# Kernel tuning notes

Measured on AMD Instinct MI355X. Metric: run time of the kernel, lower is better.

## Reference

```python
import jax, jax.numpy as jnp
import numpy as np

B, C, H, W = 256, 200, 32, 32


def setup_inputs() -> dict:
    key = jax.random.key(0)
    x = jax.random.normal(key, (B, C, H, W), dtype=jnp.float32)
    # exact init of the torch nn.Parameter: log(3.2 / c^2) * ones(1,1)
    temperature = jnp.log(3.2 / (C * C)) * jnp.ones((1, 1), dtype=jnp.float32)
    return {"x": x, "temperature": temperature}


def reference(x, temperature):
    b, c, h, w = x.shape
    xf = x.reshape(b, c, h * w)                     # (B, c, hw)
    # Gram matrix x @ x^T  -> (B, c, c)
    G = jnp.einsum('bcm,bdm->bcd', xf, xf)
    # diagonal of G = squared norms per band  -> (B, c)
    d = jnp.einsum('bcm,bcm->bc', xf, xf)
    # I_M @ (G*I) puts d_j in every row; (G*I) @ I_M puts d_i in every column
    dcov = d[:, None, :] + d[:, :, None] - 2.0 * G  # (B, c, c)
    dcov = jnp.maximum(dcov, 0.0)
    dcov = jnp.sqrt(jnp.exp(temperature)[0, 0] * dcov + 1e-5)
    # double centering: dcov@I_M/c = row means, I_M@dcov/c = col means,
    # I_M@dcov@I_M/c^2 = global mean (per batch element)
    row_mean = jnp.mean(dcov, axis=2, keepdims=True)
    col_mean = jnp.mean(dcov, axis=1, keepdims=True)
    tot_mean = jnp.mean(dcov, axis=(1, 2), keepdims=True)
    return -(dcov - row_mean - col_mean + tot_mean)
```

## Files before the change

### kernel.cpp

```cpp
#include <hip/hip_runtime.h>
#include <hip/hip_bf16.h>

typedef __bf16 bf16x8 __attribute__((ext_vector_type(8)));
typedef float  f32x4  __attribute__((ext_vector_type(4)));

#define C_DIM   200
#define HW_DIM  1024
#define NT      13
#define PADC    208
#define BK      64
#define NKC     16
#define ROWB    128
#define TILEB   (PADC*ROWB)
#define SLAB    (PADC*HW_DIM)

#define GLD16(gp, lp) __builtin_amdgcn_global_load_lds(                      \
    (const __attribute__((address_space(1))) unsigned int*)(gp),             \
    (__attribute__((address_space(3))) unsigned int*)(lp), 16, 0, 0)

__global__ __launch_bounds__(832, 4)
void spectral_corr_kernel(const float* __restrict__ x,
                          const float* __restrict__ temp,
                          float* __restrict__ out,
                          __hip_bfloat16* __restrict__ ws)
{
  __shared__ __align__(16) char sA[2][TILEB];
  __shared__ float d_lds[PADC];
  __shared__ float rs_lds[PADC];

  const int tid = threadIdx.x;
  const int b   = blockIdx.x;
  const int w   = tid >> 6;
  const int l   = tid & 63;
  const int g   = l >> 4;
  const int c   = l & 15;

  const float*    xb = x  + (size_t)b * (C_DIM * HW_DIM);
  __hip_bfloat16* wb = ws + (size_t)b * SLAB;

  for (int base = tid*8; base < C_DIM*HW_DIM; base += 832*8){
    float4 a0 = *(const float4*)(xb + base);
    float4 a1 = *(const float4*)(xb + base + 4);
    bf16x8 v;
    v[0]=(__bf16)a0.x; v[1]=(__bf16)a0.y; v[2]=(__bf16)a0.z; v[3]=(__bf16)a0.w;
    v[4]=(__bf16)a1.x; v[5]=(__bf16)a1.y; v[6]=(__bf16)a1.z; v[7]=(__bf16)a1.w;
    *reinterpret_cast<bf16x8*>(wb + base) = v;
  }
  __syncthreads();

  const float et = expf(temp[0]);

  const int si = l >> 3;
  const int sc = (l & 7) ^ si;
  const int i0 = 2*w, i1 = 2*w + 1;
  const __hip_bfloat16* gs0 = wb + (size_t)(8*i0 + si)*HW_DIM + sc*8;
  const __hip_bfloat16* gs1 = wb + (size_t)(8*i1 + si)*HW_DIM + sc*8;

  f32x4 acc[NT];
  #pragma unroll
  for (int j=0;j<NT;++j) acc[j] = (f32x4){0.f,0.f,0.f,0.f};

  GLD16(gs0, &sA[0][i0*1024]);
  GLD16(gs1, &sA[0][i1*1024]);
  __syncthreads();

  const int swz = (c & 7) << 4;
  const int rb0 = c*ROWB + ((     g*16) ^ swz);
  const int rb1 = c*ROWB + ((64 + g*16) ^ swz);

  for (int kc = 0; kc < NKC; ++kc){
    const char* bufc = sA[kc & 1];
    if (kc+1 < NKC){
      char* bufn = sA[(kc+1)&1];
      GLD16(gs0 + (kc+1)*BK, &bufn[i0*1024]);
      GLD16(gs1 + (kc+1)*BK, &bufn[i1*1024]);
    }
    #pragma unroll
    for (int s = 0; s < 2; ++s){
      const char* p = bufc + (s ? rb1 : rb0);
      bf16x8 fw = *reinterpret_cast<const bf16x8*>(p + w*2048);
      #pragma unroll
      for (int j = 0; j < NT; ++j){
        bf16x8 fj = *reinterpret_cast<const bf16x8*>(p + j*2048);
        acc[j] = __builtin_amdgcn_mfma_f32_16x16x32_bf16(fw, fj, acc[j], 0, 0, 0);
      }
    }
    __syncthreads();
  }

  #pragma unroll
  for (int j=0;j<NT;++j){
    if (j == w){
      #pragma unroll
      for (int i=0;i<4;++i)
        if (c == g*4 + i) d_lds[j*16 + c] = acc[j][i];
    }
  }
  __syncthreads();

  float dr[4];
  #pragma unroll
  for (int i=0;i<4;++i) dr[i] = d_lds[w*16 + g*4 + i];
  float rsum[4] = {0.f,0.f,0.f,0.f};
  #pragma unroll
  for (int j=0;j<NT;++j){
    const float dc = d_lds[j*16 + c];
    const bool cv  = (j*16 + c) < C_DIM;
    #pragma unroll
    for (int i=0;i<4;++i){
      float v = dr[i] + dc - 2.0f*acc[j][i];
      v = fmaxf(v, 0.0f);
      v = sqrtf(fmaf(et, v, 1e-5f));
      acc[j][i] = v;
      if (cv) rsum[i] += v;
    }
  }
  #pragma unroll
  for (int m=1;m<16;m<<=1){
    #pragma unroll
    for (int i=0;i<4;++i) rsum[i] += __shfl_xor(rsum[i], m, 64);
  }
  if (c == 0){
    #pragma unroll
    for (int i=0;i<4;++i) rs_lds[w*16 + g*4 + i] = rsum[i];
  }
  __syncthreads();

  float tot = 0.f;
  for (int r=0;r<C_DIM;++r) tot += rs_lds[r];
  const float inv  = 1.0f/(float)C_DIM;
  const float totm = tot*inv*inv;

  float* ob = out + b*(C_DIM*C_DIM);
  float rmr[4];
  #pragma unroll
  for (int i=0;i<4;++i) rmr[i] = rs_lds[w*16 + g*4 + i]*inv;
  #pragma unroll
  for (int j=0;j<NT;++j){
    const int col = j*16 + c;
    if (col < C_DIM){
      const float rmc = rs_lds[col]*inv;
      #pragma unroll
      for (int i=0;i<4;++i){
        const int row = w*16 + g*4 + i;
        if (row < C_DIM)
          ob[row*C_DIM + col] = rmr[i] + rmc - totm - acc[j][i];
      }
    }
  }
}

extern "C" void kernel_launch(void* const* d_in, const int* in_sizes, int n_in,
                              void* d_out, int out_size, void* d_ws, size_t ws_size,
                              hipStream_t stream) {
  const float* x    = (const float*)d_in[0];
  const float* temp = (const float*)d_in[1];
  float* out        = (float*)d_out;
  __hip_bfloat16* ws = (__hip_bfloat16*)d_ws;
  spectral_corr_kernel<<<dim3(256), dim3(832), 0, stream>>>(x, temp, out, ws);
}
```

Before: 354.0 us.

## Interleave fp32-to-bf16 conversion with the MFMA K-loop two chunks ahead

Previously the whole per-batch slab was converted from fp32 to bf16 into workspace before any matrix work began, behind one block-wide barrier. Now only the first two K-chunks are converted up front. Each loop iteration loads the fp32 data for chunk kc+2 into registers before its MFMAs, then packs and stores it to workspace after them, so global-memory latency overlaps with tensor-core compute. This raises register pressure and relies on the existing per-iteration barrier to make workspace writes visible before the later global-to-LDS loads read them.

```diff
diff --git a/kernel.cpp b/kernel.cpp
--- a/kernel.cpp
+++ b/kernel.cpp
@@ -17,6 +17,13 @@
 #define GLD16(gp, lp) __builtin_amdgcn_global_load_lds(                      \
     (const __attribute__((address_space(1))) unsigned int*)(gp),             \
     (__attribute__((address_space(3))) unsigned int*)(lp), 16, 0, 0)
+
+__device__ __forceinline__ bf16x8 pack8(float4 a, float4 b){
+  bf16x8 v;
+  v[0]=(__bf16)a.x; v[1]=(__bf16)a.y; v[2]=(__bf16)a.z; v[3]=(__bf16)a.w;
+  v[4]=(__bf16)b.x; v[5]=(__bf16)b.y; v[6]=(__bf16)b.z; v[7]=(__bf16)b.w;
+  return v;
+}
 
 __global__ __launch_bounds__(832, 4)
 void spectral_corr_kernel(const float* __restrict__ x,
@@ -38,17 +45,10 @@
   const float*    xb = x  + (size_t)b * (C_DIM * HW_DIM);
   __hip_bfloat16* wb = ws + (size_t)b * SLAB;
 
-  for (int base = tid*8; base < C_DIM*HW_DIM; base += 832*8){
-    float4 a0 = *(const float4*)(xb + base);
-    float4 a1 = *(const float4*)(xb + base + 4);
-    bf16x8 v;
-    v[0]=(__bf16)a0.x; v[1]=(__bf16)a0.y; v[2]=(__bf16)a0.z; v[3]=(__bf16)a0.w;
-    v[4]=(__bf16)a1.x; v[5]=(__bf16)a1.y; v[6]=(__bf16)a1.z; v[7]=(__bf16)a1.w;
-    *reinterpret_cast<bf16x8*>(wb + base) = v;
-  }
-  __syncthreads();
-
-  const float et = expf(temp[0]);
+  const int r_a  = tid >> 3,        c8_a = tid & 7;
+  const int s_b  = tid + 832;
+  const int r_b  = s_b >> 3,        c8_b = s_b & 7;
+  const bool vb  = (s_b < 1600);
 
   const int si = l >> 3;
   const int sc = (l & 7) ^ si;
@@ -60,9 +60,26 @@
   #pragma unroll
   for (int j=0;j<NT;++j) acc[j] = (f32x4){0.f,0.f,0.f,0.f};
 
+  #pragma unroll
+  for (int cc = 0; cc < 2; ++cc){
+    {
+      const float* p = xb + (size_t)r_a*HW_DIM + cc*BK + c8_a*8;
+      float4 f0 = *(const float4*)p, f1 = *(const float4*)(p+4);
+      *reinterpret_cast<bf16x8*>(wb + (size_t)r_a*HW_DIM + cc*BK + c8_a*8) = pack8(f0,f1);
+    }
+    if (vb){
+      const float* p = xb + (size_t)r_b*HW_DIM + cc*BK + c8_b*8;
+      float4 f0 = *(const float4*)p, f1 = *(const float4*)(p+4);
+      *reinterpret_cast<bf16x8*>(wb + (size_t)r_b*HW_DIM + cc*BK + c8_b*8) = pack8(f0,f1);
+    }
+  }
+  __syncthreads();
+
   GLD16(gs0, &sA[0][i0*1024]);
   GLD16(gs1, &sA[0][i1*1024]);
   __syncthreads();
+
+  const float et = expf(temp[0]);
 
   const int swz = (c & 7) << 4;
   const int rb0 = c*ROWB + ((     g*16) ^ swz);
@@ -75,6 +92,16 @@
       GLD16(gs0 + (kc+1)*BK, &bufn[i0*1024]);
       GLD16(gs1 + (kc+1)*BK, &bufn[i1*1024]);
     }
+    float4 fa0, fa1, fb0, fb1;
+    const bool cv = (kc+2 < NKC);
+    if (cv){
+      const float* pa = xb + (size_t)r_a*HW_DIM + (kc+2)*BK + c8_a*8;
+      fa0 = *(const float4*)pa; fa1 = *(const float4*)(pa+4);
+      if (vb){
+        const float* pb = xb + (size_t)r_b*HW_DIM + (kc+2)*BK + c8_b*8;
+        fb0 = *(const float4*)pb; fb1 = *(const float4*)(pb+4);
+      }
+    }
     #pragma unroll
     for (int s = 0; s < 2; ++s){
       const char* p = bufc + (s ? rb1 : rb0);
@@ -84,6 +111,11 @@
         bf16x8 fj = *reinterpret_cast<const bf16x8*>(p + j*2048);
         acc[j] = __builtin_amdgcn_mfma_f32_16x16x32_bf16(fw, fj, acc[j], 0, 0, 0);
       }
+    }
+    if (cv){
+      *reinterpret_cast<bf16x8*>(wb + (size_t)r_a*HW_DIM + (kc+2)*BK + c8_a*8) = pack8(fa0,fa1);
+      if (vb)
+        *reinterpret_cast<bf16x8*>(wb + (size_t)r_b*HW_DIM + (kc+2)*BK + c8_b*8) = pack8(fb0,fb1);
     }
     __syncthreads();
   }
@@ -105,14 +137,14 @@
   #pragma unroll
   for (int j=0;j<NT;++j){
     const float dc = d_lds[j*16 + c];
-    const bool cv  = (j*16 + c) < C_DIM;
+    const bool cvv = (j*16 + c) < C_DIM;
     #pragma unroll
     for (int i=0;i<4;++i){
       float v = dr[i] + dc - 2.0f*acc[j][i];
       v = fmaxf(v, 0.0f);
       v = sqrtf(fmaf(et, v, 1e-5f));
       acc[j][i] = v;
-      if (cv) rsum[i] += v;
+      if (cvv) rsum[i] += v;
     }
   }
   #pragma unroll
```

Result: faster. 341.6 us (-3.5%).
